# Kernel optimization log

Measured on AMD Instinct MI355X. Metric: run time of the kernel, lower is better.

The kernel has to match this reference:

```python
import jax, jax.numpy as jnp
import numpy as np

D_MODEL = 1024
N_HEADS = 16
D_FF = 4096
WINDOW = 256
EPS = 1e-5


def setup_inputs() -> dict:
    key = jax.random.key(0)
    ks = jax.random.split(key, 12)
    B, T, C = 4, 1024, D_MODEL
    s = lambda fan: 1.0 / np.sqrt(fan)
    return {
        "x": jax.random.normal(ks[0], (B, T, C), jnp.float32),
        "Wqkv": jax.random.normal(ks[1], (3 * C, C), jnp.float32) * s(C),
        "bqkv": jnp.zeros((3 * C,), jnp.float32),
        "Wo": jax.random.normal(ks[2], (C, C), jnp.float32) * s(C),
        "bo": jnp.zeros((C,), jnp.float32),
        "W1": jax.random.normal(ks[3], (D_FF, C), jnp.float32) * s(C),
        "b1": jnp.zeros((D_FF,), jnp.float32),
        "W2": jax.random.normal(ks[4], (C, D_FF), jnp.float32) * s(D_FF),
        "b2": jnp.zeros((C,), jnp.float32),
        "g1": jnp.ones((C,), jnp.float32),
        "be1": jnp.zeros((C,), jnp.float32),
        "g2": jnp.ones((C,), jnp.float32),
        "be2": jnp.zeros((C,), jnp.float32),
    }


def _layernorm(x, g, b):
    mu = jnp.mean(x, axis=-1, keepdims=True)
    var = jnp.mean(jnp.square(x - mu), axis=-1, keepdims=True)
    return (x - mu) * jax.lax.rsqrt(var + EPS) * g + b


def reference(x, Wqkv, bqkv, Wo, bo, W1, b1, W2, b2, g1, be1, g2, be2):
    B, T, C = x.shape
    H, Dh = N_HEADS, C // N_HEADS
    # QKV projection (torch MultiheadAttention packed in_proj)
    qkv = jnp.einsum("btc,ec->bte", x, Wqkv) + bqkv  # [B,T,3C]
    q, k, v = jnp.split(qkv, 3, axis=-1)
    q = q.reshape(B, T, H, Dh).transpose(0, 2, 1, 3)  # [B,H,T,Dh]
    k = k.reshape(B, T, H, Dh).transpose(0, 2, 1, 3)
    v = v.reshape(B, T, H, Dh).transpose(0, 2, 1, 3)
    scores = jnp.einsum("bhqd,bhkd->bhqk", q, k) / jnp.sqrt(jnp.float32(Dh))
    # causal banded mask: key j visible to query i iff 0 <= i-j < WINDOW
    i = jnp.arange(T)[:, None]
    j = jnp.arange(T)[None, :]
    band = (j <= i) & (i - j < WINDOW)
    scores = jnp.where(band, scores, -jnp.inf)
    attn = jax.nn.softmax(scores, axis=-1)
    ctx = jnp.einsum("bhqk,bhkd->bhqd", attn, v)  # [B,H,T,Dh]
    ctx = ctx.transpose(0, 2, 1, 3).reshape(B, T, C)
    attn_out = jnp.einsum("btc,oc->bto", ctx, Wo) + bo
    x = _layernorm(x + attn_out, g1, be1)
    h = jax.nn.gelu(jnp.einsum("btc,fc->btf", x, W1) + b1, approximate=False)
    ffn_out = jnp.einsum("btf,cf->btc", h, W2) + b2
    return _layernorm(x + ffn_out, g2, be2)
```

## Files before the change

### kernel.cpp

```cpp
#include <hip/hip_runtime.h>
#include <hip/hip_bf16.h>

typedef __attribute__((ext_vector_type(4))) float floatx4;
typedef __attribute__((ext_vector_type(8))) short shortx8;

struct bf4 { __hip_bfloat16 h[4]; };
union U8 { shortx8 v; __hip_bfloat16 h[8]; };
union U4 { unsigned long long v; __hip_bfloat16 h[4]; };

__device__ __forceinline__ void async_copy16(const __hip_bfloat16* g, __hip_bfloat16* l) {
  __builtin_amdgcn_global_load_lds((__attribute__((address_space(1))) void*)g,
                                   (__attribute__((address_space(3))) void*)l,
                                   16, 0, 0);
}

__global__ __launch_bounds__(256) void cast_all_kernel(
    const float* __restrict__ s0, __hip_bfloat16* __restrict__ d0, int nb0,
    const float* __restrict__ s1, __hip_bfloat16* __restrict__ d1, int nb1,
    const float* __restrict__ s2, __hip_bfloat16* __restrict__ d2, int nb2,
    const float* __restrict__ s3, __hip_bfloat16* __restrict__ d3, int nb3,
    const float* __restrict__ s4, __hip_bfloat16* __restrict__ d4) {
  int b = blockIdx.x;
  const float* src; __hip_bfloat16* dst;
  if (b < nb0) { src = s0; dst = d0; }
  else { b -= nb0;
    if (b < nb1) { src = s1; dst = d1; }
    else { b -= nb1;
      if (b < nb2) { src = s2; dst = d2; }
      else { b -= nb2;
        if (b < nb3) { src = s3; dst = d3; }
        else { b -= nb3; src = s4; dst = d4; }
      }
    }
  }
  const int i = b * 256 + threadIdx.x;
  const float4 v = ((const float4*)src)[i];
  bf4 o4;
  o4.h[0] = __float2bfloat16(v.x);
  o4.h[1] = __float2bfloat16(v.y);
  o4.h[2] = __float2bfloat16(v.z);
  o4.h[3] = __float2bfloat16(v.w);
  *(bf4*)(dst + (size_t)i * 4) = o4;
}

#define GEMM_SWIZZLE()                                                        \
  const int flat = blockIdx.x + gridDim.x * (blockIdx.y + 32 * blockIdx.z);   \
  const int xcd_ = flat & 7;                                                  \
  int rsw_ = flat >> 3;                                                       \
  const int mt_ = xcd_ * 4 + (rsw_ & 3);                                      \
  rsw_ >>= 2;                                                                 \
  const int nt_ = rsw_ % gridDim.x;                                           \
  const int zt_ = rsw_ / gridDim.x;

#define GEMM_STAGE(buf, koff)                                      \
  async_copy16(Ag0 + (koff),           &As[buf][tid * 8]);         \
  async_copy16(Ag0 + (koff) + rstride, &As[buf][tid * 8 + 2048]);  \
  async_copy16(Bg0 + (koff),           &Bs[buf][tid * 8]);         \
  async_copy16(Bg0 + (koff) + rstride, &Bs[buf][tid * 8 + 2048]);

#define GEMM_KLOOP(NI)                                                        \
  GEMM_STAGE(0, 0)                                                            \
  GEMM_STAGE(1, 32)                                                           \
  int cur = 0;                                                                \
  for (int it = 0; it < (NI); ++it) {                                         \
    if (it + 2 < (NI)) {                                                      \
      const int nb = (cur >= 1) ? cur - 1 : cur + 2;           \
      GEMM_STAGE(nb, (it + 2) * 32)                                           \
      asm volatile("s_waitcnt vmcnt(8)" ::: "memory");                        \
    } else if (it + 1 < (NI)) {                                               \
      asm volatile("s_waitcnt vmcnt(4)" ::: "memory");                        \
    } else {                                                                  \
      asm volatile("s_waitcnt vmcnt(0)" ::: "memory");                        \
    }                                                                         \
    asm volatile("s_barrier" ::: "memory");                                   \
    const __hip_bfloat16* Ac = As[cur];                                       \
    const __hip_bfloat16* Bc = Bs[cur];                                       \
    shortx8 afr[4], bfr[4];                                                   \
    _Pragma("unroll")                                                         \
    for (int i = 0; i < 4; ++i) {                                             \
      afr[i] = *(const shortx8*)&Ac[(wr * 64 + i * 16 + fr) * 32 + sw];       \
      bfr[i] = *(const shortx8*)&Bc[(wc * 64 + i * 16 + fr) * 32 + sw];       \
    }                                                                         \
    _Pragma("unroll")                                                         \
    for (int mi = 0; mi < 4; ++mi)                                            \
      _Pragma("unroll")                                                       \
      for (int ni = 0; ni < 4; ++ni)                                          \
        acc[mi][ni] = __builtin_amdgcn_mfma_f32_16x16x32_bf16(                \
            afr[mi], bfr[ni], acc[mi][ni], 0, 0, 0);                          \
    asm volatile("s_barrier" ::: "memory");                                   \
    cur = (cur == 2) ? 0 : cur + 1;                                           \
  }

template<int EPI>
__global__ __launch_bounds__(256) void gemm_bt(
    const __hip_bfloat16* __restrict__ A,
    const __hip_bfloat16* __restrict__ B,
    const float* __restrict__ bias,
    __hip_bfloat16* __restrict__ outb,
    int M, int N, int K)
{
  __shared__ __align__(16) __hip_bfloat16 As[3][128 * 32];
  __shared__ __align__(16) __hip_bfloat16 Bs[3][128 * 32];
  const int tid  = threadIdx.x;
  const int lane = tid & 63;
  const int wave = tid >> 6;
  const int wr = wave >> 1, wc = wave & 1;
  GEMM_SWIZZLE()
  const long bm = (long)mt_ * 128, bn = (long)nt_ * 128;
  (void)zt_;

  const int srow = tid >> 2;
  const int scol = ((((tid & 3) - (tid >> 3)) & 3) << 3);
  const __hip_bfloat16* Ag0 = A + (bm + srow) * (long)K + scol;
  const __hip_bfloat16* Bg0 = B + (bn + srow) * (long)K + scol;
  const long rstride = 64l * K;

  const int fr = lane & 15;
  const int fq = lane >> 4;
  const int sw = (((fq + ((fr >> 1) & 3)) & 3) << 3);

  const floatx4 zero = {0.f, 0.f, 0.f, 0.f};
  floatx4 acc[4][4];
#pragma unroll
  for (int mi = 0; mi < 4; ++mi)
#pragma unroll
    for (int ni = 0; ni < 4; ++ni) acc[mi][ni] = zero;

  const int NI = K >> 5;
  GEMM_KLOOP(NI)

#pragma unroll
  for (int mi = 0; mi < 4; ++mi) {
#pragma unroll
    for (int ni = 0; ni < 4; ++ni) {
      const long col = bn + wc * 64 + ni * 16 + fr;
      const float bv = bias[col];
#pragma unroll
      for (int r = 0; r < 4; ++r) {
        const long row = bm + wr * 64 + mi * 16 + fq * 4 + r;
        float v = acc[mi][ni][r] + bv;
        if (EPI == 1) {
          const float u = v + 0.044715f * v * v * v;
          v = v / (1.0f + __expf(-1.5957691216057308f * u));
        }
        outb[(size_t)row * N + col] = __float2bfloat16(v);
      }
    }
  }
}

__global__ __launch_bounds__(256) void gemm_bt_splitk(
    const __hip_bfloat16* __restrict__ A,
    const __hip_bfloat16* __restrict__ B,
    __hip_bfloat16* __restrict__ part,
    int M, int N, int K, int Klen)
{
  __shared__ __align__(16) __hip_bfloat16 As[3][128 * 32];
  __shared__ __align__(16) __hip_bfloat16 Bs[3][128 * 32];
  const int tid  = threadIdx.x;
  const int lane = tid & 63;
  const int wave = tid >> 6;
  const int wr = wave >> 1, wc = wave & 1;
  GEMM_SWIZZLE()
  const long bm = (long)mt_ * 128, bn = (long)nt_ * 128;
  const int kstart = zt_ * Klen;

  const int srow = tid >> 2;
  const int scol = ((((tid & 3) - (tid >> 3)) & 3) << 3);
  const __hip_bfloat16* Ag0 = A + (bm + srow) * (long)K + kstart + scol;
  const __hip_bfloat16* Bg0 = B + (bn + srow) * (long)K + kstart + scol;
  const long rstride = 64l * K;

  const int fr = lane & 15;
  const int fq = lane >> 4;
  const int sw = (((fq + ((fr >> 1) & 3)) & 3) << 3);

  const floatx4 zero = {0.f, 0.f, 0.f, 0.f};
  floatx4 acc[4][4];
#pragma unroll
  for (int mi = 0; mi < 4; ++mi)
#pragma unroll
    for (int ni = 0; ni < 4; ++ni) acc[mi][ni] = zero;

  const int NI = Klen >> 5;
  GEMM_KLOOP(NI)

  __hip_bfloat16* outp = part + (size_t)zt_ * M * N;
#pragma unroll
  for (int mi = 0; mi < 4; ++mi) {
#pragma unroll
    for (int ni = 0; ni < 4; ++ni) {
      const long col = bn + wc * 64 + ni * 16 + fr;
#pragma unroll
      for (int r = 0; r < 4; ++r) {
        const long row = bm + wr * 64 + mi * 16 + fq * 4 + r;
        outp[(size_t)row * N + col] = __float2bfloat16(acc[mi][ni][r]);
      }
    }
  }
}

__global__ __launch_bounds__(256) void transpose_v_kernel(
    const __hip_bfloat16* __restrict__ qkv, __hip_bfloat16* __restrict__ vt)
{
  const int bh = blockIdx.y;
  const int tt = blockIdx.x;
  const int b = bh >> 4, h = bh & 15;
  __shared__ __hip_bfloat16 tile[64][65];
  const int tid = threadIdx.x;
  const int r = tid >> 2;
  const int c = (tid & 3) << 4;
  const __hip_bfloat16* src = qkv + (size_t)(b * 1024 + tt * 64 + r) * 3072 + 2048 + h * 64 + c;
  U8 u0, u1;
  u0.v = *(const shortx8*)src;
  u1.v = *(const shortx8*)(src + 8);
#pragma unroll
  for (int j = 0; j < 8; ++j) { tile[r][c + j] = u0.h[j]; tile[r][c + 8 + j] = u1.h[j]; }
  __syncthreads();
  U8 w0, w1;
#pragma unroll
  for (int j = 0; j < 8; ++j) { w0.h[j] = tile[c + j][r]; w1.h[j] = tile[c + 8 + j][r]; }
  __hip_bfloat16* dst = vt + ((size_t)bh * 64 + r) * 1024 + tt * 64 + c;
  *(shortx8*)dst       = w0.v;
  *(shortx8*)(dst + 8) = w1.v;
}

__global__ __launch_bounds__(256) void attn_kernel(
    const __hip_bfloat16* __restrict__ qkv,
    const __hip_bfloat16* __restrict__ vt,
    __hip_bfloat16* __restrict__ ctx)
{
  const int wave = threadIdx.x >> 6;
  const int lane = threadIdx.x & 63;
  const int gw = blockIdx.x * 4 + wave;
  const int qt = gw & 63;
  const int bh = gw >> 6;
  const int b = bh >> 4, h = bh & 15;
  const int fr = lane & 15, fq = lane >> 4;
  const int q0 = qt << 4;

  __shared__ __align__(16) __hip_bfloat16 Plds[4][16 * 32];
  __hip_bfloat16* Pw = Plds[wave];

  const __hip_bfloat16* qrow = qkv + (size_t)(b * 1024 + q0 + fr) * 3072 + h * 64;
  const shortx8 aq0 = *(const shortx8*)(qrow + fq * 8);
  const shortx8 aq1 = *(const shortx8*)(qrow + 32 + fq * 8);

  const float SC = 0.125f * 1.44269504088896f;
  float m_r[4] = {-1e30f, -1e30f, -1e30f, -1e30f};
  float l_r[4] = {0.f, 0.f, 0.f, 0.f};
  const floatx4 zero = {0.f, 0.f, 0.f, 0.f};
  floatx4 o[4];
#pragma unroll
  for (int nd = 0; nd < 4; ++nd) o[nd] = zero;

  const int kt0 = (q0 >= 255) ? ((q0 - 255) >> 5) : 0;
  const int kt1 = (q0 + 15) >> 5;
  for (int kt = kt0; kt <= kt1; ++kt) {
    const int kbase = kt << 5;
    const __hip_bfloat16* krow0 = qkv + (size_t)(b * 1024 + kbase + fr) * 3072 + 1024 + h * 64;
    const __hip_bfloat16* krow1 = krow0 + 16 * 3072;
    const shortx8 bk00 = *(const shortx8*)(krow0 + fq * 8);
    const shortx8 bk01 = *(const shortx8*)(krow0 + 32 + fq * 8);
    const shortx8 bk10 = *(const shortx8*)(krow1 + fq * 8);
    const shortx8 bk11 = *(const shortx8*)(krow1 + 32 + fq * 8);
    floatx4 s0 = zero, s1 = zero;
    s0 = __builtin_amdgcn_mfma_f32_16x16x32_bf16(aq0, bk00, s0, 0, 0, 0);
    s0 = __builtin_amdgcn_mfma_f32_16x16x32_bf16(aq1, bk01, s0, 0, 0, 0);
    s1 = __builtin_amdgcn_mfma_f32_16x16x32_bf16(aq0, bk10, s1, 0, 0, 0);
    s1 = __builtin_amdgcn_mfma_f32_16x16x32_bf16(aq1, bk11, s1, 0, 0, 0);
#pragma unroll
    for (int r = 0; r < 4; ++r) { s0[r] *= SC; s1[r] *= SC; }
    if (kbase + 31 > q0 || kbase < q0 - 240) {
#pragma unroll
      for (int r = 0; r < 4; ++r) {
        const int tq = q0 + fq * 4 + r;
        const int j0 = kbase + fr;
        const int j1 = j0 + 16;
        if (j0 > tq || j0 < tq - 255) s0[r] = -3e38f;
        if (j1 > tq || j1 < tq - 255) s1[r] = -3e38f;
      }
    }
#pragma unroll
    for (int r = 0; r < 4; ++r) {
      float vmax = fmaxf(s0[r], s1[r]);
      vmax = fmaxf(vmax, __shfl_xor(vmax, 1));
      vmax = fmaxf(vmax, __shfl_xor(vmax, 2));
      vmax = fmaxf(vmax, __shfl_xor(vmax, 4));
      vmax = fmaxf(vmax, __shfl_xor(vmax, 8));
      const float mnew = fmaxf(m_r[r], vmax);
      const float alpha = exp2f(m_r[r] - mnew);
      const float p0 = exp2f(s0[r] - mnew);
      const float p1 = exp2f(s1[r] - mnew);
      m_r[r] = mnew;
      float ps = p0 + p1;
      ps += __shfl_xor(ps, 1);
      ps += __shfl_xor(ps, 2);
      ps += __shfl_xor(ps, 4);
      ps += __shfl_xor(ps, 8);
      l_r[r] = l_r[r] * alpha + ps;
      o[0][r] *= alpha; o[1][r] *= alpha; o[2][r] *= alpha; o[3][r] *= alpha;
      Pw[(fq * 4 + r) * 32 + fr]      = __float2bfloat16(p0);
      Pw[(fq * 4 + r) * 32 + 16 + fr] = __float2bfloat16(p1);
    }
    asm volatile("s_waitcnt lgkmcnt(0)" ::: "memory");
    const shortx8 ap = *(const shortx8*)&Pw[fr * 32 + fq * 8];
#pragma unroll
    for (int nd = 0; nd < 4; ++nd) {
      const shortx8 bv = *(const shortx8*)&vt[((size_t)bh * 64 + nd * 16 + fr) * 1024 + kbase + fq * 8];
      o[nd] = __builtin_amdgcn_mfma_f32_16x16x32_bf16(ap, bv, o[nd], 0, 0, 0);
    }
    asm volatile("s_waitcnt lgkmcnt(0)" ::: "memory");
  }
#pragma unroll
  for (int nd = 0; nd < 4; ++nd)
#pragma unroll
    for (int r = 0; r < 4; ++r)
      ctx[(size_t)(b * 1024 + q0 + fq * 4 + r) * 1024 + h * 64 + nd * 16 + fr] =
          __float2bfloat16(o[nd][r] / l_r[r]);
}

template<int S, int WB>
__global__ __launch_bounds__(256) void ln_sum_kernel(
    const __hip_bfloat16* __restrict__ part,
    const float* __restrict__ resid,
    const float* __restrict__ bias,
    const float* __restrict__ g, const float* __restrict__ be,
    float* __restrict__ outf, __hip_bfloat16* __restrict__ outb)
{
  const int row = blockIdx.x;
  const int tid = threadIdx.x;
  const size_t base = (size_t)row * 1024;
  float4 v = ((const float4*)(resid + base))[tid];
  const float4 bv = ((const float4*)bias)[tid];
  v.x += bv.x; v.y += bv.y; v.z += bv.z; v.w += bv.w;
#pragma unroll
  for (int s = 0; s < S; ++s) {
    U4 p;
    p.v = *(const unsigned long long*)&part[(size_t)s * 4096 * 1024 + base + tid * 4];
    v.x += __bfloat162float(p.h[0]);
    v.y += __bfloat162float(p.h[1]);
    v.z += __bfloat162float(p.h[2]);
    v.w += __bfloat162float(p.h[3]);
  }
  float sm = v.x + v.y + v.z + v.w;
  float ss = v.x * v.x + v.y * v.y + v.z * v.z + v.w * v.w;
#pragma unroll
  for (int off = 1; off < 64; off <<= 1) {
    sm += __shfl_xor(sm, off);
    ss += __shfl_xor(ss, off);
  }
  __shared__ float red[8];
  if ((tid & 63) == 0) { red[tid >> 6] = sm; red[4 + (tid >> 6)] = ss; }
  __syncthreads();
  sm = red[0] + red[1] + red[2] + red[3];
  ss = red[4] + red[5] + red[6] + red[7];
  const float mu = sm * (1.0f / 1024.0f);
  const float rs = rsqrtf(ss * (1.0f / 1024.0f) - mu * mu + 1e-5f);
  const float4 gg = ((const float4*)g)[tid];
  const float4 bb = ((const float4*)be)[tid];
  float4 y;
  y.x = (v.x - mu) * rs * gg.x + bb.x;
  y.y = (v.y - mu) * rs * gg.y + bb.y;
  y.z = (v.z - mu) * rs * gg.z + bb.z;
  y.w = (v.w - mu) * rs * gg.w + bb.w;
  ((float4*)(outf + base))[tid] = y;
  if (WB) {
    bf4 o4;
    o4.h[0] = __float2bfloat16(y.x);
    o4.h[1] = __float2bfloat16(y.y);
    o4.h[2] = __float2bfloat16(y.z);
    o4.h[3] = __float2bfloat16(y.w);
    *(bf4*)(outb + base + tid * 4) = o4;
  }
}

extern "C" void kernel_launch(void* const* d_in, const int* in_sizes, int n_in,
                              void* d_out, int out_size, void* d_ws, size_t ws_size,
                              hipStream_t stream) {
  const float* x    = (const float*)d_in[0];
  const float* Wqkv = (const float*)d_in[1];
  const float* bqkv = (const float*)d_in[2];
  const float* Wo   = (const float*)d_in[3];
  const float* bo   = (const float*)d_in[4];
  const float* W1   = (const float*)d_in[5];
  const float* b1   = (const float*)d_in[6];
  const float* W2   = (const float*)d_in[7];
  const float* b2   = (const float*)d_in[8];
  const float* g1   = (const float*)d_in[9];
  const float* be1  = (const float*)d_in[10];
  const float* g2   = (const float*)d_in[11];
  const float* be2  = (const float*)d_in[12];

  char* ws = (char*)d_ws;
  size_t off = 0;
  auto alloc = [&](size_t bytes) -> void* {
    void* p = ws + off;
    off += (bytes + 255) & ~(size_t)255;
    return p;
  };
  __hip_bfloat16* wqkvb = (__hip_bfloat16*)alloc(6291456);
  __hip_bfloat16* wob   = (__hip_bfloat16*)alloc(2097152);
  __hip_bfloat16* w1b   = (__hip_bfloat16*)alloc(8388608);
  __hip_bfloat16* w2b   = (__hip_bfloat16*)alloc(8388608);
  __hip_bfloat16* xb    = (__hip_bfloat16*)alloc(8388608);
  __hip_bfloat16* qkvb  = (__hip_bfloat16*)alloc(25165824);
  __hip_bfloat16* vtb   = (__hip_bfloat16*)alloc(8388608);
  __hip_bfloat16* ctxb  = (__hip_bfloat16*)alloc(8388608);
  __hip_bfloat16* part  = (__hip_bfloat16*)alloc(4u * 8388608);
  float*          x1f   = (float*)alloc(16777216);
  __hip_bfloat16* x1b   = (__hip_bfloat16*)alloc(8388608);
  __hip_bfloat16* hb    = (__hip_bfloat16*)alloc(33554432);
  (void)ws_size; (void)in_sizes; (void)n_in; (void)out_size;

  cast_all_kernel<<<16384, 256, 0, stream>>>(x, xb, 4096,
                                             Wqkv, wqkvb, 3072,
                                             Wo, wob, 1024,
                                             W1, w1b, 4096,
                                             W2, w2b);
  gemm_bt<0><<<dim3(24, 32), 256, 0, stream>>>(xb, wqkvb, bqkv, qkvb, 4096, 3072, 1024);
  transpose_v_kernel<<<dim3(16, 64), 256, 0, stream>>>(qkvb, vtb);
  attn_kernel<<<1024, 256, 0, stream>>>(qkvb, vtb, ctxb);
  gemm_bt_splitk<<<dim3(8, 32, 2), 256, 0, stream>>>(ctxb, wob, part, 4096, 1024, 1024, 512);
  ln_sum_kernel<2, 1><<<4096, 256, 0, stream>>>(part, x, bo, g1, be1, x1f, x1b);
  gemm_bt<1><<<dim3(32, 32), 256, 0, stream>>>(x1b, w1b, b1, hb, 4096, 4096, 1024);
  gemm_bt_splitk<<<dim3(8, 32, 4), 256, 0, stream>>>(hb, w2b, part, 4096, 1024, 4096, 1024);
  ln_sum_kernel<4, 0><<<4096, 256, 0, stream>>>(part, x1f, b2, g2, be2, (float*)d_out, nullptr);
}
```

Before: 353.1 us.

## Replace 128x128 QKV and FFN1 GEMMs with 256x256-tile 8-wave pipelined kernel

Adds a gemm256 kernel that computes 256x256 output tiles with 512 threads. It uses a 4-slot LDS ring of 32-wide K sub-tiles, so global-to-LDS copies overlap MFMA phases, and it raises wave priority around the MFMA blocks. The QKV projection and the first FFN GEMM now use it instead of the 128x128 gemm_bt, which raises arithmetic intensity per tile and reduces global loads. The trade-off is fewer workgroups (192 and 256 for a large CU count), higher register and LDS use per block (128 KB LDS), and a more fragile hand-tuned wait/barrier schedule.

```diff
diff --git a/kernel.cpp b/kernel.cpp
--- a/kernel.cpp
+++ b/kernel.cpp
@@ -43,6 +43,140 @@
   *(bf4*)(dst + (size_t)i * 4) = o4;
 }
 
+#define STG_A(slot, kt, ks)                                                    \
+  async_copy16(Ag + (size_t)(kt) * 64 + (size_t)(ks) * 32,                     \
+               &As[slot][tid * 8]);                                            \
+  async_copy16(Ag + (size_t)128 * K + (size_t)(kt) * 64 + (size_t)(ks) * 32,   \
+               &As[slot][4096 + tid * 8]);
+
+#define STG_B(slot, kt, ks)                                                    \
+  async_copy16(Bg + (size_t)(kt) * 64 + (size_t)(ks) * 32,                     \
+               &Bs[slot][tid * 8]);                                            \
+  async_copy16(Bg + (size_t)128 * K + (size_t)(kt) * 64 + (size_t)(ks) * 32,   \
+               &Bs[slot][4096 + tid * 8]);
+
+#define G256_PHASE(SLOT, MH, BLOAD, STAGE_CODE, WAIT_CODE)                     \
+  {                                                                            \
+    const __hip_bfloat16* Asl = As[SLOT];                                      \
+    const __hip_bfloat16* Bsl = Bs[SLOT];                                      \
+    if (BLOAD) {                                                               \
+      _Pragma("unroll")                                                        \
+      for (int ni = 0; ni < 4; ++ni)                                           \
+        bfr[ni] = *(const shortx8*)&Bsl[brd + ni * 512];                       \
+    }                                                                          \
+    shortx8 afr[4];                                                            \
+    _Pragma("unroll")                                                          \
+    for (int mi4 = 0; mi4 < 4; ++mi4)                                          \
+      afr[mi4] = *(const shortx8*)&Asl[ard + ((MH) * 4 + mi4) * 512];          \
+    STAGE_CODE;                                                                \
+    WAIT_CODE;                                                                 \
+    __builtin_amdgcn_s_barrier();                                              \
+    asm volatile("s_waitcnt lgkmcnt(0)" ::: "memory");                         \
+    __builtin_amdgcn_sched_barrier(0);                                         \
+    __builtin_amdgcn_s_setprio(1);                                             \
+    _Pragma("unroll")                                                          \
+    for (int mi4 = 0; mi4 < 4; ++mi4)                                          \
+      _Pragma("unroll")                                                        \
+      for (int ni = 0; ni < 4; ++ni)                                           \
+        acc[(MH) * 4 + mi4][ni] = __builtin_amdgcn_mfma_f32_16x16x32_bf16(     \
+            afr[mi4], bfr[ni], acc[(MH) * 4 + mi4][ni], 0, 0, 0);              \
+    __builtin_amdgcn_s_setprio(0);                                             \
+    __builtin_amdgcn_s_barrier();                                              \
+  }
+
+template<int EPI>
+__global__ __launch_bounds__(512, 2) void gemm256(
+    const __hip_bfloat16* __restrict__ A,
+    const __hip_bfloat16* __restrict__ B,
+    const float* __restrict__ bias,
+    __hip_bfloat16* __restrict__ outb,
+    int M, int N, int K, int NT)
+{
+  __shared__ __align__(16) __hip_bfloat16 As[4][256 * 32];
+  __shared__ __align__(16) __hip_bfloat16 Bs[4][256 * 32];
+  const int tid  = threadIdx.x;
+  const int lane = tid & 63;
+  const int wave = tid >> 6;
+  const int wr = wave >> 2;
+  const int wc = wave & 3;
+  const int fr = lane & 15;
+  const int fq = lane >> 4;
+
+  const int nwg = gridDim.x;
+  const int cpx = nwg >> 3;
+  const int swz = (blockIdx.x & 7) * cpx + (blockIdx.x >> 3);
+  const int mt = swz / NT, nt = swz % NT;
+  const long bm = (long)mt * 256, bn = (long)nt * 256;
+
+  const int srow = tid >> 2;
+  const int sch  = (tid & 3) ^ ((tid >> 3) & 3);
+  const __hip_bfloat16* Ag = A + (bm + srow) * (size_t)K + sch * 8;
+  const __hip_bfloat16* Bg = B + (bn + srow) * (size_t)K + sch * 8;
+
+  const int swc = (fq ^ ((fr >> 1) & 3)) << 3;
+  const int ard = (wr * 128 + fr) * 32 + swc;
+  const int brd = (wc * 64 + fr) * 32 + swc;
+
+  const floatx4 zero = {0.f, 0.f, 0.f, 0.f};
+  floatx4 acc[8][4];
+#pragma unroll
+  for (int mi = 0; mi < 8; ++mi)
+#pragma unroll
+    for (int ni = 0; ni < 4; ++ni) acc[mi][ni] = zero;
+
+  const int NKT = K >> 6;
+
+  STG_A(0, 0, 0) STG_B(0, 0, 0)
+  STG_A(1, 0, 1) STG_B(1, 0, 1)
+  STG_A(2, 1, 0) STG_B(2, 1, 0)
+  asm volatile("s_waitcnt vmcnt(8)" ::: "memory");
+  __builtin_amdgcn_s_barrier();
+
+  shortx8 bfr[4];
+  for (int T = 0; T < NKT; ++T) {
+    const int s00 = (2 * T) & 3;
+    const int s01 = (2 * T + 1) & 3;
+    const int sn1 = (2 * T + 3) & 3;
+    const int sn0 = (2 * T + 4) & 3;
+    const bool st1 = (T + 1 < NKT);
+    const bool st2 = (T + 2 < NKT);
+
+    G256_PHASE(s00, 0, true,
+               { if (st1) { STG_A(sn1, T + 1, 1) } },
+               {})
+    G256_PHASE(s00, 1, false,
+               { if (st1) { STG_B(sn1, T + 1, 1) } },
+               { if (st1) { asm volatile("s_waitcnt vmcnt(8)" ::: "memory"); }
+                 else     { asm volatile("s_waitcnt vmcnt(0)" ::: "memory"); } })
+    G256_PHASE(s01, 0, true,
+               { if (st2) { STG_A(sn0, T + 2, 0) } },
+               {})
+    G256_PHASE(s01, 1, false,
+               { if (st2) { STG_B(sn0, T + 2, 0) } },
+               { if (st2)      { asm volatile("s_waitcnt vmcnt(8)" ::: "memory"); }
+                 else if (st1) { asm volatile("s_waitcnt vmcnt(4)" ::: "memory"); } })
+  }
+
+#pragma unroll
+  for (int mi = 0; mi < 8; ++mi) {
+#pragma unroll
+    for (int ni = 0; ni < 4; ++ni) {
+      const long col = bn + wc * 64 + ni * 16 + fr;
+      const float bv = bias[col];
+#pragma unroll
+      for (int r = 0; r < 4; ++r) {
+        const long row = bm + wr * 128 + mi * 16 + fq * 4 + r;
+        float v = acc[mi][ni][r] + bv;
+        if (EPI == 1) {
+          const float u = v + 0.044715f * v * v * v;
+          v = v / (1.0f + __expf(-1.5957691216057308f * u));
+        }
+        outb[(size_t)row * N + col] = __float2bfloat16(v);
+      }
+    }
+  }
+}
+
 #define GEMM_SWIZZLE()                                                        \
   const int flat = blockIdx.x + gridDim.x * (blockIdx.y + 32 * blockIdx.z);   \
   const int xcd_ = flat & 7;                                                  \
@@ -53,10 +187,10 @@
   const int zt_ = rsw_ / gridDim.x;
 
 #define GEMM_STAGE(buf, koff)                                      \
-  async_copy16(Ag0 + (koff),           &As[buf][tid * 8]);         \
-  async_copy16(Ag0 + (koff) + rstride, &As[buf][tid * 8 + 2048]);  \
-  async_copy16(Bg0 + (koff),           &Bs[buf][tid * 8]);         \
-  async_copy16(Bg0 + (koff) + rstride, &Bs[buf][tid * 8 + 2048]);
+  async_copy16(Ag0 + (koff),           &Asl[buf][tid * 8]);        \
+  async_copy16(Ag0 + (koff) + rstride, &Asl[buf][tid * 8 + 2048]); \
+  async_copy16(Bg0 + (koff),           &Bsl[buf][tid * 8]);        \
+  async_copy16(Bg0 + (koff) + rstride, &Bsl[buf][tid * 8 + 2048]);
 
 #define GEMM_KLOOP(NI)                                                        \
   GEMM_STAGE(0, 0)                                                            \
@@ -73,8 +207,8 @@
       asm volatile("s_waitcnt vmcnt(0)" ::: "memory");                        \
     }                                                                         \
     asm volatile("s_barrier" ::: "memory");                                   \
-    const __hip_bfloat16* Ac = As[cur];                                       \
-    const __hip_bfloat16* Bc = Bs[cur];                                       \
+    const __hip_bfloat16* Ac = Asl[cur];                                      \
+    const __hip_bfloat16* Bc = Bsl[cur];                                      \
     shortx8 afr[4], bfr[4];                                                   \
     _Pragma("unroll")                                                         \
     for (int i = 0; i < 4; ++i) {                                             \
@@ -91,72 +225,14 @@
     cur = (cur == 2) ? 0 : cur + 1;                                           \
   }
 
-template<int EPI>
-__global__ __launch_bounds__(256) void gemm_bt(
-    const __hip_bfloat16* __restrict__ A,
-    const __hip_bfloat16* __restrict__ B,
-    const float* __restrict__ bias,
-    __hip_bfloat16* __restrict__ outb,
-    int M, int N, int K)
-{
-  __shared__ __align__(16) __hip_bfloat16 As[3][128 * 32];
-  __shared__ __align__(16) __hip_bfloat16 Bs[3][128 * 32];
-  const int tid  = threadIdx.x;
-  const int lane = tid & 63;
-  const int wave = tid >> 6;
-  const int wr = wave >> 1, wc = wave & 1;
-  GEMM_SWIZZLE()
-  const long bm = (long)mt_ * 128, bn = (long)nt_ * 128;
-  (void)zt_;
-
-  const int srow = tid >> 2;
-  const int scol = ((((tid & 3) - (tid >> 3)) & 3) << 3);
-  const __hip_bfloat16* Ag0 = A + (bm + srow) * (long)K + scol;
-  const __hip_bfloat16* Bg0 = B + (bn + srow) * (long)K + scol;
-  const long rstride = 64l * K;
-
-  const int fr = lane & 15;
-  const int fq = lane >> 4;
-  const int sw = (((fq + ((fr >> 1) & 3)) & 3) << 3);
-
-  const floatx4 zero = {0.f, 0.f, 0.f, 0.f};
-  floatx4 acc[4][4];
-#pragma unroll
-  for (int mi = 0; mi < 4; ++mi)
-#pragma unroll
-    for (int ni = 0; ni < 4; ++ni) acc[mi][ni] = zero;
-
-  const int NI = K >> 5;
-  GEMM_KLOOP(NI)
-
-#pragma unroll
-  for (int mi = 0; mi < 4; ++mi) {
-#pragma unroll
-    for (int ni = 0; ni < 4; ++ni) {
-      const long col = bn + wc * 64 + ni * 16 + fr;
-      const float bv = bias[col];
-#pragma unroll
-      for (int r = 0; r < 4; ++r) {
-        const long row = bm + wr * 64 + mi * 16 + fq * 4 + r;
-        float v = acc[mi][ni][r] + bv;
-        if (EPI == 1) {
-          const float u = v + 0.044715f * v * v * v;
-          v = v / (1.0f + __expf(-1.5957691216057308f * u));
-        }
-        outb[(size_t)row * N + col] = __float2bfloat16(v);
-      }
-    }
-  }
-}
-
 __global__ __launch_bounds__(256) void gemm_bt_splitk(
     const __hip_bfloat16* __restrict__ A,
     const __hip_bfloat16* __restrict__ B,
     __hip_bfloat16* __restrict__ part,
     int M, int N, int K, int Klen)
 {
-  __shared__ __align__(16) __hip_bfloat16 As[3][128 * 32];
-  __shared__ __align__(16) __hip_bfloat16 Bs[3][128 * 32];
+  __shared__ __align__(16) __hip_bfloat16 Asl[3][128 * 32];
+  __shared__ __align__(16) __hip_bfloat16 Bsl[3][128 * 32];
   const int tid  = threadIdx.x;
   const int lane = tid & 63;
   const int wave = tid >> 6;
@@ -418,12 +494,12 @@
                                              Wo, wob, 1024,
                                              W1, w1b, 4096,
                                              W2, w2b);
-  gemm_bt<0><<<dim3(24, 32), 256, 0, stream>>>(xb, wqkvb, bqkv, qkvb, 4096, 3072, 1024);
+  gemm256<0><<<192, 512, 0, stream>>>(xb, wqkvb, bqkv, qkvb, 4096, 3072, 1024, 12);
   transpose_v_kernel<<<dim3(16, 64), 256, 0, stream>>>(qkvb, vtb);
   attn_kernel<<<1024, 256, 0, stream>>>(qkvb, vtb, ctxb);
   gemm_bt_splitk<<<dim3(8, 32, 2), 256, 0, stream>>>(ctxb, wob, part, 4096, 1024, 1024, 512);
   ln_sum_kernel<2, 1><<<4096, 256, 0, stream>>>(part, x, bo, g1, be1, x1f, x1b);
-  gemm_bt<1><<<dim3(32, 32), 256, 0, stream>>>(x1b, w1b, b1, hb, 4096, 4096, 1024);
+  gemm256<1><<<256, 512, 0, stream>>>(x1b, w1b, b1, hb, 4096, 4096, 1024, 16);
   gemm_bt_splitk<<<dim3(8, 32, 4), 256, 0, stream>>>(hb, w2b, part, 4096, 1024, 4096, 1024);
   ln_sum_kernel<4, 0><<<4096, 256, 0, stream>>>(part, x1f, b2, g2, be2, (float*)d_out, nullptr);
 }
```

Result: faster. 336.1 us (-4.8%).
